# Performance work log

Measured on AMD Instinct MI355X. Metric: run time of the kernel, lower is better.

## Reference

```python
import jax, jax.numpy as jnp
import numpy as np

DIM = 16      # must equal K*K per the module's reshape structure
K = 4         # kernel_size
HEADS = 8
SCALE = (DIM // HEADS) ** (-0.5)


def setup_inputs() -> dict:
    key = jax.random.key(0)
    k1, k2 = jax.random.split(key)
    x = jax.random.normal(k1, (2, 64, 67, 67), dtype=jnp.float32)
    # torch Linear(dim, 3*dim, bias=False) weight: [3*dim, dim]
    w_qkv = jax.random.normal(k2, (3 * DIM, DIM), dtype=jnp.float32) * 0.1
    return {"x": x, "w_qkv": w_qkv}


def reference(x, w_qkv):
    B, C, H, W = x.shape
    k = K
    Ho, Wo = H - k + 1, W - k + 1          # unfold output grid (stride=1)
    L = Ho * Wo
    # Unfold: patches[b, c, i*k+j, ph, pw] = x[b, c, ph+i, pw+j]
    # (matches torch F.unfold channel ordering c-major, then i, then j)
    patches = jnp.stack(
        [x[:, :, i:i + Ho, j:j + Wo] for i in range(k) for j in range(k)],
        axis=2,
    )  # [B, C, k*k, Ho, Wo]
    seq = L // (k * k)                      # L must be divisible by k*k
    # [B*C*k*k, seq, k*k] -- flatten (Ho,Wo)->L row-major then split into (seq, k*k)
    xu = patches.reshape(B * C * k * k, seq, k * k)
    # tiny attention over each row; feature dim = k*k = DIM
    qkv = xu @ w_qkv.T                      # [N, seq, 3*DIM]
    q, kk_, v = jnp.split(qkv, 3, axis=-1)
    scores = jnp.einsum('nqd,nkd->nqk', q, kk_) * SCALE   # [N, seq, seq]
    attn = jax.nn.softmax(scores, axis=-1)                # dropout = identity (eval)
    ao = jnp.einsum('nqk,nkd->nqd', attn, v)              # [N, seq, DIM]
    ao = ao.reshape(B, C, k, k, Ho, Wo)
    # overlap-add fold back onto the HxW grid
    out = jnp.zeros_like(x)
    for i in range(k):
        for j in range(k):
            out = out.at[:, :, i:Ho + i, j:Wo + j].add(ao[:, :, i, j])
    return out
```

## Files before the change

### kernel.cpp

```cpp
#include <hip/hip_runtime.h>


#define BATCH 2
#define CHAN 64
#define HWDIM 67
#define SEQ 256
#define DIM 16
#define OUT_TOTAL (BATCH * CHAN * HWDIM * HWDIM)
#define ATT_SCALE 0.70710678118654752f
#define LOG2E 1.44269504088896340736f

typedef _Float16 half4 __attribute__((ext_vector_type(4)));
typedef _Float16 half8 __attribute__((ext_vector_type(8)));
typedef float float4v __attribute__((ext_vector_type(4)));
typedef __fp16 fp16x2 __attribute__((ext_vector_type(2)));
typedef unsigned int uint2v __attribute__((ext_vector_type(2)));

static __device__ __forceinline__ half4 mk_half4(float a, float b, float c, float d) {
    fp16x2 lo = __builtin_amdgcn_cvt_pkrtz(a, b);
    fp16x2 hi = __builtin_amdgcn_cvt_pkrtz(c, d);
    uint2v u;
    u[0] = __builtin_bit_cast(unsigned int, lo);
    u[1] = __builtin_bit_cast(unsigned int, hi);
    return __builtin_bit_cast(half4, u);
}

static __device__ __forceinline__ half4 pack4(float4v c) {
    return mk_half4(c[0], c[1], c[2], c[3]);
}

static __device__ __forceinline__ void att_step(const half4 vf, const float4v sfr,
                                                float& l, float4v& oacc) {
    const float p0 = __builtin_amdgcn_exp2f(sfr[0]);
    const float p1 = __builtin_amdgcn_exp2f(sfr[1]);
    const float p2 = __builtin_amdgcn_exp2f(sfr[2]);
    const float p3 = __builtin_amdgcn_exp2f(sfr[3]);
    l += (p0 + p1) + (p2 + p3);
    const half4 pb = mk_half4(p0, p1, p2, p3);
    oacc = __builtin_amdgcn_mfma_f32_16x16x16f16(vf, pb, oacc, 0, 0, 0);
}

__global__ __launch_bounds__(512, 4) void ska_fused(
    const float* __restrict__ x,
    const float* __restrict__ w,
    float* __restrict__ out)
{
    __shared__ __align__(16) _Float16 buf[2][16][64][8];
    __shared__ float fold[64][69];

    const int b  = (int)(blockIdx.x & 7) * 64 + (int)(blockIdx.x >> 3);
    const int bc = b >> 2;
    const int ii = b & 3;

    const int tid  = threadIdx.x;
    const int wave = tid >> 6;
    const int lane = tid & 63;
    const int o = lane & 15;
    const int g = lane >> 4;

    {
        float* ff = &fold[0][0];
        for (int i = tid; i < 64 * 69; i += 512) ff[i] = 0.f;
    }

    const float4 wq4 = *(const float4*)(w + ( 0 + o) * DIM + 4 * g);
    const float4 wk4 = *(const float4*)(w + (16 + o) * DIM + 4 * g);
    const float4 wv4 = *(const float4*)(w + (32 + o) * DIM + 4 * g);
    const half4 wqf = mk_half4(wq4.x * (ATT_SCALE * LOG2E), wq4.y * (ATT_SCALE * LOG2E),
                               wq4.z * (ATT_SCALE * LOG2E), wq4.w * (ATT_SCALE * LOG2E));
    const half4 wkf = mk_half4(wk4.x, wk4.y, wk4.z, wk4.w);
    const half4 wvf = mk_half4(wv4.x, wv4.y, wv4.z, wv4.w);

    const float4v zf = (float4v){0.f, 0.f, 0.f, 0.f};

    const float* xb = x + ((size_t)bc * HWDIM + ii) * HWDIM + (o & 3) * 16 + 4 * g;
    const int roff0 = (8 * wave + (o >> 2)) * HWDIM;
    const int roff1 = roff0 + 4 * HWDIM;

    float xr0a = xb[roff0 + 0], xr0b = xb[roff0 + 1],
          xr0c = xb[roff0 + 2], xr0d = xb[roff0 + 3];
    float xr1a = xb[roff1 + 0], xr1b = xb[roff1 + 1],
          xr1c = xb[roff1 + 2], xr1d = xb[roff1 + 3];

    for (int jj = 0; jj < 4; ++jj) {
        const int cur = jj & 1;

        half4 qfr0, qfr1;
        {
            const half4 xf0 = mk_half4(xr0a, xr0b, xr0c, xr0d);
            const half4 kf0 = pack4(__builtin_amdgcn_mfma_f32_16x16x16f16(wkf, xf0, zf, 0, 0, 0));
            const half4 vf0 = pack4(__builtin_amdgcn_mfma_f32_16x16x16f16(xf0, wvf, zf, 0, 0, 0));
            *(half8*)&buf[cur][2 * wave][lane][0] =
                __builtin_shufflevector(kf0, vf0, 0, 1, 2, 3, 4, 5, 6, 7);
            qfr0 = pack4(__builtin_amdgcn_mfma_f32_16x16x16f16(wqf, xf0, zf, 0, 0, 0));

            const half4 xf1 = mk_half4(xr1a, xr1b, xr1c, xr1d);
            const half4 kf1 = pack4(__builtin_amdgcn_mfma_f32_16x16x16f16(wkf, xf1, zf, 0, 0, 0));
            const half4 vf1 = pack4(__builtin_amdgcn_mfma_f32_16x16x16f16(xf1, wvf, zf, 0, 0, 0));
            *(half8*)&buf[cur][2 * wave + 1][lane][0] =
                __builtin_shufflevector(kf1, vf1, 0, 1, 2, 3, 4, 5, 6, 7);
            qfr1 = pack4(__builtin_amdgcn_mfma_f32_16x16x16f16(wqf, xf1, zf, 0, 0, 0));
        }

        if (jj < 3) {
            const int d = jj + 1;
            xr0a = xb[roff0 + d + 0]; xr0b = xb[roff0 + d + 1];
            xr0c = xb[roff0 + d + 2]; xr0d = xb[roff0 + d + 3];
            xr1a = xb[roff1 + d + 0]; xr1b = xb[roff1 + d + 1];
            xr1c = xb[roff1 + d + 2]; xr1d = xb[roff1 + d + 3];
        }

        __syncthreads();

        float4v oacc0 = zf, oacc1 = zf;
        float l0 = 0.f, l1 = 0.f;

        half8 kvc = *(const half8*)&buf[cur][0][lane][0];
#pragma unroll 4
        for (int t = 0; t < 16; ++t) {
            const half8 kvn = *(const half8*)&buf[cur][(t + 1) & 15][lane][0];
            const half4 kf = __builtin_shufflevector(kvc, kvc, 0, 1, 2, 3);
            const half4 vf = __builtin_shufflevector(kvc, kvc, 4, 5, 6, 7);
            const float4v s0 = __builtin_amdgcn_mfma_f32_16x16x16f16(kf, qfr0, zf, 0, 0, 0);
            const float4v s1 = __builtin_amdgcn_mfma_f32_16x16x16f16(kf, qfr1, zf, 0, 0, 0);
            att_step(vf, s0, l0, oacc0);
            att_step(vf, s1, l1, oacc1);
            kvc = kvn;
        }

#pragma unroll
        for (int u = 0; u < 2; ++u) {
            float lj = u ? l1 : l0;
            lj += __shfl_xor(lj, 16, 64);
            lj += __shfl_xor(lj, 32, 64);
            const float rl = __builtin_amdgcn_rcpf(lj);
            const float4v oa = u ? oacc1 : oacc0;
            const int r = 8 * wave + 4 * u + (o >> 2);
            const int c = 16 * (o & 3) + 4 * g + jj;
            fold[r][c + 0] += oa[0] * rl;
            fold[r][c + 1] += oa[1] * rl;
            fold[r][c + 2] += oa[2] * rl;
            fold[r][c + 3] += oa[3] * rl;
        }
    }

    __syncthreads();

    float* ob = out + ((size_t)bc * HWDIM + ii) * HWDIM;
    for (int i = tid; i < 64 * HWDIM; i += 512) {
        const int r = i / HWDIM;
        const int c = i % HWDIM;
        atomicAdd(&ob[r * HWDIM + c], fold[r][c]);
    }
}

extern "C" void kernel_launch(void* const* d_in, const int* in_sizes, int n_in,
                              void* d_out, int out_size, void* d_ws, size_t ws_size,
                              hipStream_t stream) {
    const float* x = (const float*)d_in[0];
    const float* w = (const float*)d_in[1];
    float* out = (float*)d_out;
    (void)d_ws; (void)ws_size; (void)in_sizes; (void)n_in;

    (void)hipMemsetAsync(out, 0, (size_t)out_size * sizeof(float), stream);
    ska_fused<<<BATCH * CHAN * 4, 512, 0, stream>>>(x, w, out);
}
```

Before: 80.79 us.

## Split attention into workspace kernel plus gather-sum fold kernel, removing atomics

```diff
diff --git a/kernel.cpp b/kernel.cpp
--- a/kernel.cpp
+++ b/kernel.cpp
@@ -4,8 +4,8 @@
 #define BATCH 2
 #define CHAN 64
 #define HWDIM 67
-#define SEQ 256
 #define DIM 16
+#define PLANE 4096
 #define OUT_TOTAL (BATCH * CHAN * HWDIM * HWDIM)
 #define ATT_SCALE 0.70710678118654752f
 #define LOG2E 1.44269504088896340736f
@@ -40,13 +40,12 @@
     oacc = __builtin_amdgcn_mfma_f32_16x16x16f16(vf, pb, oacc, 0, 0, 0);
 }
 
-__global__ __launch_bounds__(512, 4) void ska_fused(
+__global__ __launch_bounds__(256, 4) void ska_attn(
     const float* __restrict__ x,
     const float* __restrict__ w,
-    float* __restrict__ out)
+    _Float16* __restrict__ ao)
 {
-    __shared__ __align__(16) _Float16 buf[2][16][64][8];
-    __shared__ float fold[64][69];
+    __shared__ __align__(16) _Float16 qlds[4][16][64][4];
 
     const int b  = (int)(blockIdx.x & 7) * 64 + (int)(blockIdx.x >> 3);
     const int bc = b >> 2;
@@ -57,11 +56,7 @@
     const int lane = tid & 63;
     const int o = lane & 15;
     const int g = lane >> 4;
-
-    {
-        float* ff = &fold[0][0];
-        for (int i = tid; i < 64 * 69; i += 512) ff[i] = 0.f;
-    }
+    const int jj = wave;
 
     const float4 wq4 = *(const float4*)(w + ( 0 + o) * DIM + 4 * g);
     const float4 wk4 = *(const float4*)(w + (16 + o) * DIM + 4 * g);
@@ -73,6 +68,105 @@
 
     const float4v zf = (float4v){0.f, 0.f, 0.f, 0.f};
 
+    const float* xb = x + ((size_t)bc * HWDIM + ii) * HWDIM + (o & 3) * 16 + 4 * g + jj;
+    half4 kf[16], vf[16];
+#pragma unroll
+    for (int t = 0; t < 16; ++t) {
+        const float* xp = xb + (4 * t + (o >> 2)) * HWDIM;
+        const half4 xf = mk_half4(xp[0], xp[1], xp[2], xp[3]);
+        kf[t] = pack4(__builtin_amdgcn_mfma_f32_16x16x16f16(wkf, xf, zf, 0, 0, 0));
+        vf[t] = pack4(__builtin_amdgcn_mfma_f32_16x16x16f16(xf, wvf, zf, 0, 0, 0));
+        const half4 qf = pack4(__builtin_amdgcn_mfma_f32_16x16x16f16(wqf, xf, zf, 0, 0, 0));
+        *(half4*)&qlds[wave][t][lane][0] = qf;
+    }
+
+    const int n = bc * 16 + ii * 4 + jj;
+    _Float16* aop = ao + (size_t)n * PLANE;
+
+    for (int jq = 0; jq < 16; jq += 2) {
+        const half4 qp0 = *(const half4*)&qlds[wave][jq][lane][0];
+        const half4 qp1 = *(const half4*)&qlds[wave][jq + 1][lane][0];
+        float4v oacc0 = zf, oacc1 = zf;
+        float l0 = 0.f, l1 = 0.f;
+#pragma unroll
+        for (int t = 0; t < 16; ++t) {
+            const float4v s0 = __builtin_amdgcn_mfma_f32_16x16x16f16(kf[t], qp0, zf, 0, 0, 0);
+            const float4v s1 = __builtin_amdgcn_mfma_f32_16x16x16f16(kf[t], qp1, zf, 0, 0, 0);
+            att_step(vf[t], s0, l0, oacc0);
+            att_step(vf[t], s1, l1, oacc1);
+        }
+#pragma unroll
+        for (int u = 0; u < 2; ++u) {
+            float lj = u ? l1 : l0;
+            lj += __shfl_xor(lj, 16, 64);
+            lj += __shfl_xor(lj, 32, 64);
+            const float rl = __builtin_amdgcn_rcpf(lj);
+            const float4v oa = u ? oacc1 : oacc0;
+            const int query = (jq + u) * 16 + o;
+            *(half4*)(aop + query * DIM + 4 * g) =
+                mk_half4(oa[0] * rl, oa[1] * rl, oa[2] * rl, oa[3] * rl);
+        }
+    }
+}
+
+__global__ __launch_bounds__(256) void ska_sum(
+    const _Float16* __restrict__ ao,
+    float* __restrict__ out)
+{
+    const int idx = (int)(blockIdx.x * 256 + threadIdx.x);
+    if (idx >= OUT_TOTAL) return;
+    const int bc  = idx / (HWDIM * HWDIM);
+    const int rem = idx % (HWDIM * HWDIM);
+    const int h   = rem / HWDIM;
+    const int ww  = rem % HWDIM;
+    float acc = 0.f;
+#pragma unroll
+    for (int i = 0; i < 4; ++i) {
+        const int hp = h - i;
+        if (hp < 0 || hp >= 64) continue;
+#pragma unroll
+        for (int j = 0; j < 4; ++j) {
+            const int wp = ww - j;
+            if (wp < 0 || wp >= 64) continue;
+            const int n = bc * 16 + i * 4 + j;
+            const int q = (hp << 2) + (wp >> 4);
+            const int d = wp & 15;
+            acc += (float)ao[(size_t)n * PLANE + q * DIM + d];
+        }
+    }
+    out[idx] = acc;
+}
+
+__global__ __launch_bounds__(512, 4) void ska_fused_atomic(
+    const float* __restrict__ x, const float* __restrict__ w,
+    float* __restrict__ out)
+{
+    __shared__ __align__(16) _Float16 buf[2][16][64][8];
+    __shared__ float fold[64][69];
+
+    const int b  = (int)(blockIdx.x & 7) * 64 + (int)(blockIdx.x >> 3);
+    const int bc = b >> 2;
+    const int ii = b & 3;
+    const int tid  = threadIdx.x;
+    const int wave = tid >> 6;
+    const int lane = tid & 63;
+    const int o = lane & 15;
+    const int g = lane >> 4;
+
+    {
+        float* ff = &fold[0][0];
+        for (int i = tid; i < 64 * 69; i += 512) ff[i] = 0.f;
+    }
+
+    const float4 wq4 = *(const float4*)(w + ( 0 + o) * DIM + 4 * g);
+    const float4 wk4 = *(const float4*)(w + (16 + o) * DIM + 4 * g);
+    const float4 wv4 = *(const float4*)(w + (32 + o) * DIM + 4 * g);
+    const half4 wqf = mk_half4(wq4.x * (ATT_SCALE * LOG2E), wq4.y * (ATT_SCALE * LOG2E),
+                               wq4.z * (ATT_SCALE * LOG2E), wq4.w * (ATT_SCALE * LOG2E));
+    const half4 wkf = mk_half4(wk4.x, wk4.y, wk4.z, wk4.w);
+    const half4 wvf = mk_half4(wv4.x, wv4.y, wv4.z, wv4.w);
+    const float4v zf = (float4v){0.f, 0.f, 0.f, 0.f};
+
     const float* xb = x + ((size_t)bc * HWDIM + ii) * HWDIM + (o & 3) * 16 + 4 * g;
     const int roff0 = (8 * wave + (o >> 2)) * HWDIM;
     const int roff1 = roff0 + 4 * HWDIM;
@@ -84,7 +178,6 @@
 
     for (int jj = 0; jj < 4; ++jj) {
         const int cur = jj & 1;
-
         half4 qfr0, qfr1;
         {
             const half4 xf0 = mk_half4(xr0a, xr0b, xr0c, xr0d);
@@ -93,7 +186,6 @@
             *(half8*)&buf[cur][2 * wave][lane][0] =
                 __builtin_shufflevector(kf0, vf0, 0, 1, 2, 3, 4, 5, 6, 7);
             qfr0 = pack4(__builtin_amdgcn_mfma_f32_16x16x16f16(wqf, xf0, zf, 0, 0, 0));
-
             const half4 xf1 = mk_half4(xr1a, xr1b, xr1c, xr1d);
             const half4 kf1 = pack4(__builtin_amdgcn_mfma_f32_16x16x16f16(wkf, xf1, zf, 0, 0, 0));
             const half4 vf1 = pack4(__builtin_amdgcn_mfma_f32_16x16x16f16(xf1, wvf, zf, 0, 0, 0));
@@ -101,7 +193,6 @@
                 __builtin_shufflevector(kf1, vf1, 0, 1, 2, 3, 4, 5, 6, 7);
             qfr1 = pack4(__builtin_amdgcn_mfma_f32_16x16x16f16(wqf, xf1, zf, 0, 0, 0));
         }
-
         if (jj < 3) {
             const int d = jj + 1;
             xr0a = xb[roff0 + d + 0]; xr0b = xb[roff0 + d + 1];
@@ -109,12 +200,10 @@
             xr1a = xb[roff1 + d + 0]; xr1b = xb[roff1 + d + 1];
             xr1c = xb[roff1 + d + 2]; xr1d = xb[roff1 + d + 3];
         }
-
         __syncthreads();
 
         float4v oacc0 = zf, oacc1 = zf;
         float l0 = 0.f, l1 = 0.f;
-
         half8 kvc = *(const half8*)&buf[cur][0][lane][0];
 #pragma unroll 4
         for (int t = 0; t < 16; ++t) {
@@ -127,7 +216,6 @@
             att_step(vf, s1, l1, oacc1);
             kvc = kvn;
         }
-
 #pragma unroll
         for (int u = 0; u < 2; ++u) {
             float lj = u ? l1 : l0;
@@ -143,14 +231,11 @@
             fold[r][c + 3] += oa[3] * rl;
         }
     }
-
     __syncthreads();
 
     float* ob = out + ((size_t)bc * HWDIM + ii) * HWDIM;
     for (int i = tid; i < 64 * HWDIM; i += 512) {
-        const int r = i / HWDIM;
-        const int c = i % HWDIM;
-        atomicAdd(&ob[r * HWDIM + c], fold[r][c]);
+        atomicAdd(&ob[i], fold[i / HWDIM][i % HWDIM]);
     }
 }
 
@@ -160,8 +245,15 @@
     const float* x = (const float*)d_in[0];
     const float* w = (const float*)d_in[1];
     float* out = (float*)d_out;
-    (void)d_ws; (void)ws_size; (void)in_sizes; (void)n_in;
-
-    (void)hipMemsetAsync(out, 0, (size_t)out_size * sizeof(float), stream);
-    ska_fused<<<BATCH * CHAN * 4, 512, 0, stream>>>(x, w, out);
-}
+    (void)in_sizes; (void)n_in;
+
+    const size_t need = (size_t)BATCH * CHAN * 16 * PLANE * sizeof(_Float16);
+    if (ws_size >= need) {
+        _Float16* ao = (_Float16*)d_ws;
+        ska_attn<<<BATCH * CHAN * 4, 256, 0, stream>>>(x, w, ao);
+        ska_sum<<<(OUT_TOTAL + 255) / 256, 256, 0, stream>>>(ao, out);
+    } else {
+        (void)hipMemsetAsync(out, 0, (size_t)out_size * sizeof(float), stream);
+        ska_fused_atomic<<<BATCH * CHAN * 4, 512, 0, stream>>>(x, w, out);
+    }
+}
```

Result: slower. 95.55 us (+18.3%).
